# Kernel optimization log

Hardware: AMD Instinct MI355X
Metric: run time of the kernel (lower is better)

## Reference

```python
import jax, jax.numpy as jnp
import numpy as np

N = 50000      # nodes
E = 800000     # edges (avg degree 16)
S = 2          # sample_size
D_IN = 128     # input_dim
D_NOISE = 64   # noise_dim
D0 = 256       # output_dims[0]
D1 = 256       # output_dims[1]


def setup_inputs() -> dict:
    key = jax.random.key(0)
    ks = jax.random.split(key, 8)
    X = jax.random.normal(ks[0], (1, N, D_IN), dtype=jnp.float32)
    edge_src = jax.random.randint(ks[1], (E,), 0, N)
    edge_dst = jax.random.randint(ks[2], (E,), 0, N)
    # Bernoulli(0.5) noise, as in torch.distributions.Bernoulli
    epsilon = (jax.random.uniform(ks[3], (S, N, D_NOISE)) < 0.5).astype(jnp.float32)
    W0 = jax.random.normal(ks[4], (D_IN + D_NOISE, D0), dtype=jnp.float32) * 0.05
    b0 = jnp.zeros((D0,), jnp.float32)
    W1 = jax.random.normal(ks[5], (D0, D1), dtype=jnp.float32) * 0.05
    b1 = jnp.zeros((D1,), jnp.float32)
    eps0 = jnp.zeros((), jnp.float32)  # GINConv learnable eps, init 0
    eps1 = jnp.zeros((), jnp.float32)
    return dict(X=X, epsilon=epsilon, edge_src=edge_src, edge_dst=edge_dst,
                W0=W0, b0=b0, W1=W1, b1=b1, eps0=eps0, eps1=eps1)


def reference(X, epsilon, edge_src, edge_dst, W0, b0, W1, b1, eps0, eps1):
    # Expand features over sample dim and concat noise: [S, N, D_IN + D_NOISE]
    feat = jnp.broadcast_to(X, (epsilon.shape[0], X.shape[1], X.shape[2]))
    h = jnp.concatenate([feat, epsilon], axis=2)

    def gin_layer(h, eps, W, b):
        # sum aggregation over in-edges: agg[:, d] += h[:, s] for each edge (s, d)
        agg = jnp.zeros_like(h).at[:, edge_dst, :].add(h[:, edge_src, :])
        return jax.nn.relu(((1.0 + eps) * h + agg) @ W + b)

    h = gin_layer(h, eps0, W0, b0)
    h = gin_layer(h, eps1, W1, b1)
    out = jax.nn.relu(h)  # outer activation applied once more in forward()
    return out, epsilon
```

## Files before the change

### kernel.cpp

```cpp
#include <hip/hip_runtime.h>
#include <hip/hip_bf16.h>

#define NN 50000
#define NE 800000
#define NS 2
#define DIN 128
#define DNOISE 64
#define DH0 192
#define DOUT 256
#define NB 49

typedef __bf16 bf16x8 __attribute__((ext_vector_type(8)));
typedef float floatx4 __attribute__((ext_vector_type(4)));


__device__ inline float bflo(unsigned int u) { return __uint_as_float(u << 16); }
__device__ inline float bfhi(unsigned int u) { return __uint_as_float(u & 0xffff0000u); }
__device__ inline unsigned short f2bf_bits(float x) {
    __hip_bfloat16 b = __float2bfloat16(x);
    return *reinterpret_cast<unsigned short*>(&b);
}
__device__ inline unsigned int pack2(float lo, float hi) {
    return (unsigned int)f2bf_bits(lo) | ((unsigned int)f2bf_bits(hi) << 16);
}


__global__ void count_kernel(const int* __restrict__ dst, int* __restrict__ cnt) {
    int i = blockIdx.x * blockDim.x + threadIdx.x;
    if (i < NE) atomicAdd(&cnt[dst[i]], 1);
}

__global__ __launch_bounds__(1024) void scanA_kernel(const int* __restrict__ cnt, int* __restrict__ bsum) {
    int i = blockIdx.x * 1024 + threadIdx.x;
    int v = (i < NN) ? cnt[i] : 0;
    for (int off = 32; off > 0; off >>= 1) v += __shfl_down(v, off);
    __shared__ int wsum[16];
    if ((threadIdx.x & 63) == 0) wsum[threadIdx.x >> 6] = v;
    __syncthreads();
    if (threadIdx.x == 0) {
        int s = 0;
        for (int k = 0; k < 16; ++k) s += wsum[k];
        bsum[blockIdx.x] = s;
    }
}

__global__ __launch_bounds__(64) void scanB_kernel(int* __restrict__ bsum) {
    int lane = threadIdx.x;
    int orig = (lane < NB) ? bsum[lane] : 0;
    int v = orig;
    for (int off = 1; off < 64; off <<= 1) {
        int t = __shfl_up(v, off);
        if (lane >= off) v += t;
    }
    if (lane < NB) bsum[lane] = v - orig;
}

__global__ __launch_bounds__(1024) void scanC_kernel(int* __restrict__ cnt, const int* __restrict__ bsum,
                                                     int* __restrict__ row_ptr) {
    __shared__ int buf[1024];
    int tid = threadIdx.x;
    int i = blockIdx.x * 1024 + tid;
    int v = (i < NN) ? cnt[i] : 0;
    buf[tid] = v;
    __syncthreads();
    for (int off = 1; off < 1024; off <<= 1) {
        int t = (tid >= off) ? buf[tid - off] : 0;
        __syncthreads();
        buf[tid] += t;
        __syncthreads();
    }
    int excl = buf[tid] - v + bsum[blockIdx.x];
    if (i < NN) { row_ptr[i + 1] = excl + v; cnt[i] = excl; }
    if (i == 0) row_ptr[0] = 0;
}

__global__ void fill_kernel(const int* __restrict__ src, const int* __restrict__ dst,
                            int* __restrict__ cursor, int* __restrict__ col_idx) {
    int i = blockIdx.x * blockDim.x + threadIdx.x;
    if (i < NE) {
        int p = atomicAdd(&cursor[dst[i]], 1);
        col_idx[p] = src[i];
    }
}

#define XQ (NN * DIN / 4)
#define XB4 ((XQ + 255) / 256)
#define NR_BLOCKS ((NS * NN + 255) / 256)

__global__ void prep_kernel(const float* __restrict__ X, unsigned short* __restrict__ Xb,
                            const float* __restrict__ noise, uint2* __restrict__ Nbit,
                            float* __restrict__ out_eps) {
    int b = blockIdx.x;
    if (b < XB4) {
        int i = b * 256 + threadIdx.x;
        if (i < XQ) {
            float4 v = reinterpret_cast<const float4*>(X)[i];
            ushort4 o;
            o.x = f2bf_bits(v.x); o.y = f2bf_bits(v.y); o.z = f2bf_bits(v.z); o.w = f2bf_bits(v.w);
            reinterpret_cast<ushort4*>(Xb)[i] = o;
        }
    } else {
        int r = (b - XB4) * 256 + threadIdx.x;
        if (r < NS * NN) {
            const float4* p = reinterpret_cast<const float4*>(noise + (size_t)r * DNOISE);
            float4* oe = reinterpret_cast<float4*>(out_eps + (size_t)r * DNOISE);
            unsigned int lo = 0, hi = 0;
            for (int q = 0; q < 8; ++q) {
                float4 v = p[q];
                oe[q] = v;
                int base = q * 4;
                lo |= (v.x != 0.f ? 1u : 0u) << base;
                lo |= (v.y != 0.f ? 1u : 0u) << (base + 1);
                lo |= (v.z != 0.f ? 1u : 0u) << (base + 2);
                lo |= (v.w != 0.f ? 1u : 0u) << (base + 3);
            }
            for (int q = 8; q < 16; ++q) {
                float4 v = p[q];
                oe[q] = v;
                int base = q * 4 - 32;
                hi |= (v.x != 0.f ? 1u : 0u) << base;
                hi |= (v.y != 0.f ? 1u : 0u) << (base + 1);
                hi |= (v.z != 0.f ? 1u : 0u) << (base + 2);
                hi |= (v.w != 0.f ? 1u : 0u) << (base + 3);
            }
            uint2 o; o.x = lo; o.y = hi;
            Nbit[r] = o;
        }
    }
}


__global__ void transpose_both(const float* __restrict__ W0, const float* __restrict__ W1,
                               __hip_bfloat16* __restrict__ Wt0, __hip_bfloat16* __restrict__ Wt1) {
    int b = blockIdx.x;
    if (b < DOUT) {
        for (int k = threadIdx.x; k < DH0; k += blockDim.x)
            Wt0[(size_t)b * DH0 + k] = __float2bfloat16(W0[(size_t)k * DOUT + b]);
    } else {
        int n = b - DOUT;
        for (int k = threadIdx.x; k < DOUT; k += blockDim.x)
            Wt1[(size_t)n * DOUT + k] = __float2bfloat16(W1[(size_t)k * DOUT + n]);
    }
}


__global__ __launch_bounds__(256) void agg0_kernel(
    const unsigned int* __restrict__ Xb,
    const uint2* __restrict__ Nbit,
    const int* __restrict__ row_ptr, const int* __restrict__ col_idx,
    const float* __restrict__ eps0p,
    unsigned int* __restrict__ z0) {
    const int d = blockIdx.x * 2 + (threadIdx.x >> 7);
    const int cc = threadIdx.x & 127;
    const float c = 1.f + eps0p[0];
    const int beg = row_ptr[d], end = row_ptr[d + 1];
    if (cc < 64) {
        const unsigned int* src = Xb + cc;
        unsigned int u = src[(size_t)d * 64];
        float aL = c * bflo(u), aH = c * bfhi(u);
        int e = beg;
        for (; e + 3 < end; e += 4) {
            int i0 = col_idx[e], i1 = col_idx[e + 1], i2 = col_idx[e + 2], i3 = col_idx[e + 3];
            unsigned int u0 = src[(size_t)i0 * 64], u1 = src[(size_t)i1 * 64];
            unsigned int u2 = src[(size_t)i2 * 64], u3 = src[(size_t)i3 * 64];
            aL += (bflo(u0) + bflo(u1)) + (bflo(u2) + bflo(u3));
            aH += (bfhi(u0) + bfhi(u1)) + (bfhi(u2) + bfhi(u3));
        }
        for (; e < end; ++e) {
            unsigned int ue = src[(size_t)col_idx[e] * 64];
            aL += bflo(ue); aH += bfhi(ue);
        }
        unsigned int r = pack2(aL, aH);
        z0[(size_t)d * 96 + cc] = r;
        z0[(size_t)(NN + d) * 96 + cc] = r;
    } else {
        int j = cc - 64;
        int s = j >> 5, col = j & 31;
        const uint2* src = Nbit + (size_t)s * NN;
        const int word = col >> 4;
        const int sh = (2 * col) & 31;
        uint2 uS = src[d];
        unsigned int wS = word ? uS.y : uS.x;
        int c0 = 0, c1 = 0;
        int e = beg;
        for (; e + 3 < end; e += 4) {
            uint2 u0 = src[col_idx[e]], u1 = src[col_idx[e + 1]];
            uint2 u2 = src[col_idx[e + 2]], u3 = src[col_idx[e + 3]];
            unsigned int w0 = word ? u0.y : u0.x, w1 = word ? u1.y : u1.x;
            unsigned int w2 = word ? u2.y : u2.x, w3 = word ? u3.y : u3.x;
            c0 += (int)((w0 >> sh) & 1) + (int)((w1 >> sh) & 1) + (int)((w2 >> sh) & 1) + (int)((w3 >> sh) & 1);
            c1 += (int)((w0 >> (sh + 1)) & 1) + (int)((w1 >> (sh + 1)) & 1) +
                  (int)((w2 >> (sh + 1)) & 1) + (int)((w3 >> (sh + 1)) & 1);
        }
        for (; e < end; ++e) {
            uint2 ue = src[col_idx[e]];
            unsigned int we = word ? ue.y : ue.x;
            c0 += (int)((we >> sh) & 1);
            c1 += (int)((we >> (sh + 1)) & 1);
        }
        float aL = c * (float)((wS >> sh) & 1) + (float)c0;
        float aH = c * (float)((wS >> (sh + 1)) & 1) + (float)c1;
        z0[(size_t)(s * NN + d) * 96 + 64 + col] = pack2(aL, aH);
    }
}


__global__ __launch_bounds__(256) void agg1_kernel(
    const uint2* __restrict__ h,
    const int* __restrict__ row_ptr, const int* __restrict__ col_idx,
    const float* __restrict__ eps1p,
    uint2* __restrict__ z1) {
    const int d = blockIdx.x * 2 + (threadIdx.x >> 7);
    const int s = (threadIdx.x >> 6) & 1;
    const int cc = threadIdx.x & 63;
    const float c = 1.f + eps1p[0];
    const int beg = row_ptr[d], end = row_ptr[d + 1];
    const uint2* src = h + (size_t)s * NN * 64 + cc;
    uint2 u = src[(size_t)d * 64];
    float aL0 = c * bflo(u.x), aH0 = c * bfhi(u.x);
    float aL1 = c * bflo(u.y), aH1 = c * bfhi(u.y);
    int e = beg;
    for (; e + 7 < end; e += 8) {
        uint2 g[8];
#pragma unroll
        for (int q = 0; q < 8; ++q) g[q] = src[(size_t)col_idx[e + q] * 64];
#pragma unroll
        for (int q = 0; q < 8; ++q) {
            aL0 += bflo(g[q].x); aH0 += bfhi(g[q].x);
            aL1 += bflo(g[q].y); aH1 += bfhi(g[q].y);
        }
    }
    for (; e + 3 < end; e += 4) {
        uint2 u0 = src[(size_t)col_idx[e] * 64], u1 = src[(size_t)col_idx[e + 1] * 64];
        uint2 u2 = src[(size_t)col_idx[e + 2] * 64], u3 = src[(size_t)col_idx[e + 3] * 64];
        aL0 += (bflo(u0.x) + bflo(u1.x)) + (bflo(u2.x) + bflo(u3.x));
        aH0 += (bfhi(u0.x) + bfhi(u1.x)) + (bfhi(u2.x) + bfhi(u3.x));
        aL1 += (bflo(u0.y) + bflo(u1.y)) + (bflo(u2.y) + bflo(u3.y));
        aH1 += (bfhi(u0.y) + bfhi(u1.y)) + (bfhi(u2.y) + bfhi(u3.y));
    }
    for (; e < end; ++e) {
        uint2 ue = src[(size_t)col_idx[e] * 64];
        aL0 += bflo(ue.x); aH0 += bfhi(ue.x);
        aL1 += bflo(ue.y); aH1 += bfhi(ue.y);
    }
    uint2 r; r.x = pack2(aL0, aH0); r.y = pack2(aL1, aH1);
    z1[(size_t)(s * NN + d) * 64 + cc] = r;
}


__device__ inline void store_out(float* C, size_t idx, float v) { C[idx] = v; }
__device__ inline void store_out(__hip_bfloat16* C, size_t idx, float v) { C[idx] = __float2bfloat16(v); }

template <int K, typename OUT_T>
__global__ __launch_bounds__(256) void gemm_bias_relu(
    const __hip_bfloat16* __restrict__ A, const __hip_bfloat16* __restrict__ Wt,
    const float* __restrict__ bias, OUT_T* __restrict__ C, int M) {
    __shared__ uint4 ldsbuf[512];
    char* lds = (char*)ldsbuf;

    const int p = blockIdx.x;
    const int mm = p >> 3, rr8 = p & 7;
    const int cg = mm & 3, qq = mm >> 2;
    const int rg = qq * 8 + rr8;
    const int blockRow = rg * 256;
    if (blockRow >= M) return;
    const int colBase = cg * 64;

    const int tid = threadIdx.x;
    const int lane = tid & 63;
    const int wave = tid >> 6;
    const int lo = lane & 15, quad = lane >> 4;
    const int rowBase = blockRow + wave * 64;

    const int n0 = tid >> 3, j0 = tid & 7;
    const int n1 = n0 + 32;
    const __hip_bfloat16* wg0 = Wt + (size_t)(colBase + n0) * K + j0 * 8;
    const __hip_bfloat16* wg1 = Wt + (size_t)(colBase + n1) * K + j0 * 8;
    const int lw0 = n0 * 128 + ((j0 ^ (n0 & 7)) << 4);
    const int lw1 = n1 * 128 + ((j0 ^ (n1 & 7)) << 4);

    floatx4 acc[4][4];
#pragma unroll
    for (int i = 0; i < 4; ++i)
#pragma unroll
        for (int j = 0; j < 4; ++j) acc[i][j] = (floatx4){0.f, 0.f, 0.f, 0.f};

    unsigned int aoff[4];
#pragma unroll
    for (int rt = 0; rt < 4; ++rt) {
        int rowi = rowBase + rt * 16 + lo;
        if (rowi >= M) rowi = M - 1;
        aoff[rt] = (unsigned int)rowi * (unsigned int)(K * 2);
    }
    const char* Ab = (const char*)A + quad * 16;

    const int NC = K >> 6;

    {
        uint4 s0 = *(const uint4*)wg0;
        uint4 s1 = *(const uint4*)wg1;
        *(uint4*)(lds + lw0) = s0;
        *(uint4*)(lds + lw1) = s1;
    }
    __syncthreads();

    for (int c = 0; c < NC; ++c) {
        uint4 q0 = {0, 0, 0, 0}, q1 = {0, 0, 0, 0};
        if (c + 1 < NC) {
            q0 = *(const uint4*)(wg0 + (c + 1) * 64);
            q1 = *(const uint4*)(wg1 + (c + 1) * 64);
        }
#pragma unroll
        for (int ks = 0; ks < 2; ++ks) {
            bf16x8 a[4], b[4];
            const int kbyte = c * 128 + ks * 64;
#pragma unroll
            for (int rt = 0; rt < 4; ++rt)
                a[rt] = *(const bf16x8*)(Ab + aoff[rt] + kbyte);
#pragma unroll
            for (int ct = 0; ct < 4; ++ct) {
                int nr = ct * 16 + lo;
                b[ct] = *(const bf16x8*)(lds + nr * 128 + ((((ks << 2) + quad) ^ (nr & 7)) << 4));
            }
#pragma unroll
            for (int rt = 0; rt < 4; ++rt)
#pragma unroll
                for (int ct = 0; ct < 4; ++ct)
                    acc[rt][ct] = __builtin_amdgcn_mfma_f32_16x16x32_bf16(a[rt], b[ct], acc[rt][ct], 0, 0, 0);
        }
        __syncthreads();
        if (c + 1 < NC) {
            *(uint4*)(lds + lw0) = q0;
            *(uint4*)(lds + lw1) = q1;
            __syncthreads();
        }
    }

#pragma unroll
    for (int ct = 0; ct < 4; ++ct) {
        const int col = colBase + ct * 16 + lo;
        const float bv = bias[col];
#pragma unroll
        for (int rt = 0; rt < 4; ++rt) {
#pragma unroll
            for (int r = 0; r < 4; ++r) {
                int row = rowBase + rt * 16 + quad * 4 + r;
                if (row < M) {
                    float v = acc[rt][ct][r] + bv;
                    store_out(C, (size_t)row * DOUT + col, v > 0.f ? v : 0.f);
                }
            }
        }
    }
}

#define GEMM_GRID 1568

extern "C" void kernel_launch(void* const* d_in, const int* in_sizes, int n_in,
                              void* d_out, int out_size, void* d_ws, size_t ws_size,
                              hipStream_t stream) {
    const float* X = (const float*)d_in[0];
    const float* noise = (const float*)d_in[1];
    const int* esrc = (const int*)d_in[2];
    const int* edst = (const int*)d_in[3];
    const float* W0 = (const float*)d_in[4];
    const float* b0 = (const float*)d_in[5];
    const float* W1 = (const float*)d_in[6];
    const float* b1 = (const float*)d_in[7];
    const float* eps0 = (const float*)d_in[8];
    const float* eps1 = (const float*)d_in[9];
    float* out = (float*)d_out;

    const int M = NS * NN;

    char* w = (char*)d_ws;
    auto carve = [&](size_t bytes) { char* p = w; w += (bytes + 511) & ~(size_t)511; return p; };
    int* cursor = (int*)carve((size_t)NN * 4);
    int* row_ptr = (int*)carve((size_t)(NN + 1) * 4);
    int* col_idx = (int*)carve((size_t)NE * 4);
    int* bsum = (int*)carve((size_t)NB * 4);
    uint2* Nbit = (uint2*)carve((size_t)M * 8);
    __hip_bfloat16* Wt0 = (__hip_bfloat16*)carve((size_t)DH0 * DOUT * 2);
    __hip_bfloat16* Wt1 = (__hip_bfloat16*)carve((size_t)DOUT * DOUT * 2);
    unsigned int* z = (unsigned int*)carve((size_t)M * DOUT * 2);

    __hip_bfloat16* h1 = (__hip_bfloat16*)d_out;
    unsigned short* Xb = (unsigned short*)(z + (size_t)M * 96);

    hipMemsetAsync(cursor, 0, (size_t)NN * 4, stream);
    count_kernel<<<(NE + 255) / 256, 256, 0, stream>>>(edst, cursor);
    scanA_kernel<<<NB, 1024, 0, stream>>>(cursor, bsum);
    scanB_kernel<<<1, 64, 0, stream>>>(bsum);
    scanC_kernel<<<NB, 1024, 0, stream>>>(cursor, bsum, row_ptr);
    fill_kernel<<<(NE + 255) / 256, 256, 0, stream>>>(esrc, edst, cursor, col_idx);
    prep_kernel<<<XB4 + NR_BLOCKS, 256, 0, stream>>>(X, Xb, noise, Nbit,
                                                     out + (size_t)M * DOUT);
    transpose_both<<<2 * DOUT, 256, 0, stream>>>(W0, W1, Wt0, Wt1);

    agg0_kernel<<<NN / 2, 256, 0, stream>>>(
        (const unsigned int*)Xb, Nbit, row_ptr, col_idx, eps0, z);
    gemm_bias_relu<DH0, __hip_bfloat16><<<GEMM_GRID, 256, 0, stream>>>(
        (const __hip_bfloat16*)z, Wt0, b0, h1, M);
    agg1_kernel<<<NN / 2, 256, 0, stream>>>(
        (const uint2*)h1, row_ptr, col_idx, eps1, (uint2*)z);
    gemm_bias_relu<DOUT, float><<<GEMM_GRID, 256, 0, stream>>>(
        (const __hip_bfloat16*)z, Wt1, b1, out, M);
}
```

Measured before the change: 614.5 us.

## Preload full packed weight slice into LDS and remap GEMM block order

Weights are repacked on device into an MFMA-fragment-friendly layout so each GEMM block copies its whole 64-column weight slice into LDS once. This removes the per-chunk double-buffer loop and its barriers, and the K loop is fully unrolled. The block-to-tile mapping changes so consecutive blocks are spread across row groups differently, and launch bounds request two blocks per CU. LDS use grows to 32KB for K=256, and the different traversal order changes cache locality for A rows.

```diff
diff --git a/kernel.cpp b/kernel.cpp
--- a/kernel.cpp
+++ b/kernel.cpp
@@ -130,16 +130,21 @@
 }
 
 
-__global__ void transpose_both(const float* __restrict__ W0, const float* __restrict__ W1,
-                               __hip_bfloat16* __restrict__ Wt0, __hip_bfloat16* __restrict__ Wt1) {
-    int b = blockIdx.x;
-    if (b < DOUT) {
-        for (int k = threadIdx.x; k < DH0; k += blockDim.x)
-            Wt0[(size_t)b * DH0 + k] = __float2bfloat16(W0[(size_t)k * DOUT + b]);
-    } else {
-        int n = b - DOUT;
-        for (int k = threadIdx.x; k < DOUT; k += blockDim.x)
-            Wt1[(size_t)n * DOUT + k] = __float2bfloat16(W1[(size_t)k * DOUT + n]);
+template <int K>
+__global__ void pack_w(const float* __restrict__ W, uint4* __restrict__ Wp) {
+    const int n = blockIdx.x;
+    const int tj = threadIdx.x;
+    if (tj < K / 8) {
+        unsigned short h[8];
+#pragma unroll
+        for (int r = 0; r < 8; ++r)
+            h[r] = f2bf_bits(W[(size_t)(tj * 8 + r) * DOUT + n]);
+        uint4 o;
+        o.x = (unsigned)h[0] | ((unsigned)h[1] << 16);
+        o.y = (unsigned)h[2] | ((unsigned)h[3] << 16);
+        o.z = (unsigned)h[4] | ((unsigned)h[5] << 16);
+        o.w = (unsigned)h[6] | ((unsigned)h[7] << 16);
+        Wp[(size_t)((n >> 6) * (K / 8) + tj) * 64 + (n & 63)] = o;
     }
 }
 
@@ -251,33 +256,32 @@
 __device__ inline void store_out(float* C, size_t idx, float v) { C[idx] = v; }
 __device__ inline void store_out(__hip_bfloat16* C, size_t idx, float v) { C[idx] = __float2bfloat16(v); }
 
+#define GEMM_GRID 1568
+
 template <int K, typename OUT_T>
-__global__ __launch_bounds__(256) void gemm_bias_relu(
-    const __hip_bfloat16* __restrict__ A, const __hip_bfloat16* __restrict__ Wt,
+__global__ __launch_bounds__(256, 2) void gemm_bias_relu(
+    const __hip_bfloat16* __restrict__ A, const uint4* __restrict__ Wp,
     const float* __restrict__ bias, OUT_T* __restrict__ C, int M) {
-    __shared__ uint4 ldsbuf[512];
-    char* lds = (char*)ldsbuf;
+    constexpr int NJ = K / 8;
+    __shared__ uint4 lds[NJ * 64];
 
     const int p = blockIdx.x;
-    const int mm = p >> 3, rr8 = p & 7;
-    const int cg = mm & 3, qq = mm >> 2;
-    const int rg = qq * 8 + rr8;
+    const int l = (p & 7) * (GEMM_GRID / 8) + (p >> 3);
+    const int cg = l & 3;
+    const int rg = l >> 2;
     const int blockRow = rg * 256;
     if (blockRow >= M) return;
-    const int colBase = cg * 64;
 
     const int tid = threadIdx.x;
-    const int lane = tid & 63;
-    const int wave = tid >> 6;
+    const uint4* wsrc = Wp + (size_t)cg * (NJ * 64);
+#pragma unroll
+    for (int i = 0; i < NJ / 4; ++i)
+        lds[i * 256 + tid] = wsrc[i * 256 + tid];
+    __syncthreads();
+
+    const int lane = tid & 63, wave = tid >> 6;
     const int lo = lane & 15, quad = lane >> 4;
     const int rowBase = blockRow + wave * 64;
-
-    const int n0 = tid >> 3, j0 = tid & 7;
-    const int n1 = n0 + 32;
-    const __hip_bfloat16* wg0 = Wt + (size_t)(colBase + n0) * K + j0 * 8;
-    const __hip_bfloat16* wg1 = Wt + (size_t)(colBase + n1) * K + j0 * 8;
-    const int lw0 = n0 * 128 + ((j0 ^ (n0 & 7)) << 4);
-    const int lw1 = n1 * 128 + ((j0 ^ (n1 & 7)) << 4);
 
     floatx4 acc[4][4];
 #pragma unroll
@@ -294,51 +298,25 @@
     }
     const char* Ab = (const char*)A + quad * 16;
 
-    const int NC = K >> 6;
-
-    {
-        uint4 s0 = *(const uint4*)wg0;
-        uint4 s1 = *(const uint4*)wg1;
-        *(uint4*)(lds + lw0) = s0;
-        *(uint4*)(lds + lw1) = s1;
-    }
-    __syncthreads();
-
-    for (int c = 0; c < NC; ++c) {
-        uint4 q0 = {0, 0, 0, 0}, q1 = {0, 0, 0, 0};
-        if (c + 1 < NC) {
-            q0 = *(const uint4*)(wg0 + (c + 1) * 64);
-            q1 = *(const uint4*)(wg1 + (c + 1) * 64);
-        }
-#pragma unroll
-        for (int ks = 0; ks < 2; ++ks) {
-            bf16x8 a[4], b[4];
-            const int kbyte = c * 128 + ks * 64;
-#pragma unroll
-            for (int rt = 0; rt < 4; ++rt)
-                a[rt] = *(const bf16x8*)(Ab + aoff[rt] + kbyte);
-#pragma unroll
-            for (int ct = 0; ct < 4; ++ct) {
-                int nr = ct * 16 + lo;
-                b[ct] = *(const bf16x8*)(lds + nr * 128 + ((((ks << 2) + quad) ^ (nr & 7)) << 4));
-            }
-#pragma unroll
-            for (int rt = 0; rt < 4; ++rt)
-#pragma unroll
-                for (int ct = 0; ct < 4; ++ct)
-                    acc[rt][ct] = __builtin_amdgcn_mfma_f32_16x16x32_bf16(a[rt], b[ct], acc[rt][ct], 0, 0, 0);
-        }
-        __syncthreads();
-        if (c + 1 < NC) {
-            *(uint4*)(lds + lw0) = q0;
-            *(uint4*)(lds + lw1) = q1;
-            __syncthreads();
-        }
+#pragma unroll
+    for (int ks = 0; ks < K / 32; ++ks) {
+        bf16x8 a[4], b[4];
+#pragma unroll
+        for (int rt = 0; rt < 4; ++rt)
+            a[rt] = *(const bf16x8*)(Ab + aoff[rt] + ks * 64);
+#pragma unroll
+        for (int ct = 0; ct < 4; ++ct)
+            b[ct] = *(const bf16x8*)&lds[(ks * 4 + quad) * 64 + ct * 16 + lo];
+#pragma unroll
+        for (int rt = 0; rt < 4; ++rt)
+#pragma unroll
+            for (int ct = 0; ct < 4; ++ct)
+                acc[rt][ct] = __builtin_amdgcn_mfma_f32_16x16x32_bf16(a[rt], b[ct], acc[rt][ct], 0, 0, 0);
     }
 
 #pragma unroll
     for (int ct = 0; ct < 4; ++ct) {
-        const int col = colBase + ct * 16 + lo;
+        const int col = cg * 64 + ct * 16 + lo;
         const float bv = bias[col];
 #pragma unroll
         for (int rt = 0; rt < 4; ++rt) {
@@ -353,8 +331,6 @@
         }
     }
 }
-
-#define GEMM_GRID 1568
 
 extern "C" void kernel_launch(void* const* d_in, const int* in_sizes, int n_in,
                               void* d_out, int out_size, void* d_ws, size_t ws_size,
@@ -380,8 +356,8 @@
     int* col_idx = (int*)carve((size_t)NE * 4);
     int* bsum = (int*)carve((size_t)NB * 4);
     uint2* Nbit = (uint2*)carve((size_t)M * 8);
-    __hip_bfloat16* Wt0 = (__hip_bfloat16*)carve((size_t)DH0 * DOUT * 2);
-    __hip_bfloat16* Wt1 = (__hip_bfloat16*)carve((size_t)DOUT * DOUT * 2);
+    uint4* Wp0 = (uint4*)carve((size_t)DH0 * DOUT * 2);
+    uint4* Wp1 = (uint4*)carve((size_t)DOUT * DOUT * 2);
     unsigned int* z = (unsigned int*)carve((size_t)M * DOUT * 2);
 
     __hip_bfloat16* h1 = (__hip_bfloat16*)d_out;
@@ -395,14 +371,15 @@
     fill_kernel<<<(NE + 255) / 256, 256, 0, stream>>>(esrc, edst, cursor, col_idx);
     prep_kernel<<<XB4 + NR_BLOCKS, 256, 0, stream>>>(X, Xb, noise, Nbit,
                                                      out + (size_t)M * DOUT);
-    transpose_both<<<2 * DOUT, 256, 0, stream>>>(W0, W1, Wt0, Wt1);
+    pack_w<DH0><<<DOUT, 64, 0, stream>>>(W0, Wp0);
+    pack_w<DOUT><<<DOUT, 64, 0, stream>>>(W1, Wp1);
 
     agg0_kernel<<<NN / 2, 256, 0, stream>>>(
         (const unsigned int*)Xb, Nbit, row_ptr, col_idx, eps0, z);
     gemm_bias_relu<DH0, __hip_bfloat16><<<GEMM_GRID, 256, 0, stream>>>(
-        (const __hip_bfloat16*)z, Wt0, b0, h1, M);
+        (const __hip_bfloat16*)z, Wp0, b0, h1, M);
     agg1_kernel<<<NN / 2, 256, 0, stream>>>(
         (const uint2*)h1, row_ptr, col_idx, eps1, (uint2*)z);
     gemm_bias_relu<DOUT, float><<<GEMM_GRID, 256, 0, stream>>>(
-        (const __hip_bfloat16*)z, Wt1, b1, out, M);
-}
+        (const __hip_bfloat16*)z, Wp1, b1, out, M);
+}
```

Result: no change. 616.4 us (+0.3%).
